# Optimization experiments

Measured on AMD Instinct MI355X. Metric: run time of the kernel, lower is better.

The kernel has to match this reference:

```python
import jax, jax.numpy as jnp
import numpy as np

N = 100000      # nodes
E = 320000      # edges
D = 128         # num_node_in_embeddings
DE = 256        # num_edge_in_embeddings = 2*D
NOBJ = 160
NREL = 27
BN_EPS = 1e-5   # eval-mode BatchNorm with running_mean=0, running_var=1


def setup_inputs() -> dict:
    key = jax.random.key(0)
    ks = jax.random.split(key, 24)
    f32 = jnp.float32
    def rn(k, shape, scale=0.05):
        return jax.random.normal(k, shape, f32) * scale
    return {
        "node_feats": jax.random.normal(ks[0], (N, D), f32),
        "edge_index": jax.random.randint(ks[1], (E, 2), 0, N),
        # GCNConv layers (W: [in,out], bias)
        "gcn1_W": rn(ks[2], (D, D // 2)), "gcn1_b": rn(ks[3], (D // 2,)),
        "gcn2_W": rn(ks[4], (D // 2, D)), "gcn2_b": rn(ks[5], (D,)),
        # edge attention (Linear(DE, D//2))
        "eattn_W": rn(ks[6], (DE, D // 2)), "eattn_b": rn(ks[7], (D // 2,)),
        # node attention (Linear(D, DE//2)) and indicator reduction (Linear(DE, DE//2))
        "nattn_W": rn(ks[8], (D, DE // 2)), "nattn_b": rn(ks[9], (DE // 2,)),
        "nred_W": rn(ks[10], (DE, DE // 2)), "nred_b": rn(ks[11], (DE // 2,)),
        # edge MLPs (1x1 Conv1d == Linear)
        "emlp1_W": rn(ks[12], (DE, DE // 2)), "emlp1_b": rn(ks[13], (DE // 2,)),
        "emlp2_W": rn(ks[14], (DE // 2, DE)), "emlp2_b": rn(ks[15], (DE,)),
        # node classification head
        "nlin1_W": rn(ks[16], (D, D // 2)),
        "nbn_g": jnp.ones((D // 2,), f32) + rn(ks[17], (D // 2,)),
        "nbn_b": rn(ks[18], (D // 2,)),
        "nlin2_W": rn(ks[19], (D // 2, NOBJ)),
        # edge classification head
        "elin1_W": rn(ks[20], (DE, DE // 2)),
        "ebn_g": jnp.ones((DE // 2,), f32) + rn(ks[21], (DE // 2,)),
        "ebn_b": rn(ks[22], (DE // 2,)),
        "elin2_W": rn(ks[23], (DE // 2, NREL)),
    }


def _seg_mean(vals, idx, n):
    # torch_scatter 'mean': sum / clamp(count, 1)
    s = jax.ops.segment_sum(vals, idx, num_segments=n)
    c = jax.ops.segment_sum(jnp.ones((vals.shape[0], 1), vals.dtype), idx, num_segments=n)
    return s / jnp.maximum(c, 1.0)


def _gcn_conv(x, src, dst, W, b, n):
    # PyG GCNConv, add_self_loops=True, symmetric normalization.
    lin = x @ W
    deg = jax.ops.segment_sum(jnp.ones((src.shape[0],), x.dtype), dst, num_segments=n) + 1.0
    dis = jax.lax.rsqrt(deg)                       # deg^{-1/2}, includes self-loop
    norm = dis[src] * dis[dst]                     # per-edge norm
    agg = jax.ops.segment_sum(lin[src] * norm[:, None], dst, num_segments=n)
    return agg + lin * (dis * dis)[:, None] + b    # self-loop term + bias


def _bn_eval(x, g, b):
    # eval-mode BatchNorm1d with running_mean=0, running_var=1
    return x * (g / jnp.sqrt(1.0 + BN_EPS)) + b


def reference(node_feats, edge_index, gcn1_W, gcn1_b, gcn2_W, gcn2_b,
              eattn_W, eattn_b, nattn_W, nattn_b, nred_W, nred_b,
              emlp1_W, emlp1_b, emlp2_W, emlp2_b,
              nlin1_W, nbn_g, nbn_b, nlin2_W,
              elin1_W, ebn_g, ebn_b, elin2_W):
    n = node_feats.shape[0]
    src = edge_index[:, 0]
    dst = edge_index[:, 1]

    # edge feature init: [subject, object - subject]  -> [E, DE]
    subj = node_feats[src]
    edge_feats = jnp.concatenate([subj, node_feats[dst] - subj], axis=1)

    # edge attention -> scatter-mean indicators over rows/cols -> node gate
    edge_ind = edge_feats @ eattn_W + eattn_b            # [E, D/2]
    row = _seg_mean(edge_ind, src, n)                    # [N, D/2]
    col = _seg_mean(edge_ind, dst, n)                    # [N, D/2]
    agg_edge_indicator = jax.nn.sigmoid(row * col)

    # two GCN layers (dropout is identity in eval mode)
    h = jax.nn.relu(_gcn_conv(node_feats, src, dst, gcn1_W, gcn1_b, n)) * agg_edge_indicator
    h = jax.nn.relu(_gcn_conv(h, src, dst, gcn2_W, gcn2_b, n))           # [N, D]

    # node attention -> per-edge gate
    node_ind = jax.nn.relu(h @ nattn_W + nattn_b)                        # [N, DE/2]
    econcat = jnp.concatenate([node_ind[src], node_ind[dst]], axis=1)    # [E, DE]
    agg_node_indicator = jax.nn.sigmoid(econcat @ nred_W + nred_b)       # [E, DE/2]

    # edge MLPs (1x1 convs == linears over edges)
    ef = jax.nn.relu(edge_feats @ emlp1_W + emlp1_b) * agg_node_indicator
    ef = jax.nn.relu(ef @ emlp2_W + emlp2_b)                             # [E, DE]

    # node head: linear -> BN(eval) -> leaky_relu(0.2) -> linear -> softmax over classes
    nx = jax.nn.leaky_relu(_bn_eval(h @ nlin1_W, nbn_g, nbn_b), 0.2)
    node_logits = jax.nn.softmax(nx @ nlin2_W, axis=1)                   # [N, NOBJ]

    # edge head: note original applies softmax on dim=1 of [1,E,NREL] -> over EDGES
    ex = jax.nn.leaky_relu(_bn_eval(ef @ elin1_W, ebn_g, ebn_b), 0.2)
    edge_logits = jax.nn.softmax(ex @ elin2_W, axis=0)                   # [E, NREL]

    return (node_logits, edge_logits)
```

## Files before the change

kernel.cpp:

```cpp
#include <hip/hip_runtime.h>

#define NN 100000
#define EE 320000

typedef unsigned int uint32;
typedef __attribute__((ext_vector_type(8))) short bf16x8;
typedef __attribute__((ext_vector_type(4))) float f32x4;
typedef __attribute__((ext_vector_type(16))) float f32x16;

__device__ __forceinline__ float4 ld4(const float* p){ return *(const float4*)p; }
__device__ __forceinline__ void st4(float* p, const float4 v){ *(float4*)p = v; }
__device__ __forceinline__ float sigm(float x){ return 1.f/(1.f + expf(-x)); }
__device__ __forceinline__ short f2b(float f){
  union { float f; uint32 u; } v; v.f = f;
  uint32 r = (v.u + 0x7FFFu + ((v.u>>16)&1u)) >> 16;
  return (short)r;
}
__device__ __forceinline__ float b2f(short s){
  union { uint32 u; float f; } v; v.u = ((uint32)(unsigned short)s) << 16; return v.f;
}

constexpr int EM_STORE=0, EM_BRELU=1, EM_BNLK=2;

template<int K,int NOUT,int EM>
__global__ __launch_bounds__(256) void gemm_k(
    const float* __restrict__ A,
    const float* __restrict__ W, const float* __restrict__ bias,
    const float* __restrict__ bng,
    float* __restrict__ C, int M)
{
  constexpr int CN = NOUT/16;
  __shared__ float As[16][68];
  __shared__ float Ws[16][NOUT];
  const int t  = threadIdx.x;
  const int tx = t & 15, ty = t >> 4;
  const int row0 = blockIdx.x * 64;

  float acc[4][CN];
  #pragma unroll
  for (int i=0;i<4;i++)
    #pragma unroll
    for (int j=0;j<CN;j++) acc[i][j]=0.f;

  const int r_st  = t >> 2;
  const int kq_st = (t & 3) * 4;

  for (int k0=0;k0<K;k0+=16) {
    {
      float4 v = make_float4(0.f,0.f,0.f,0.f);
      const int gr = row0 + r_st;
      if (gr < M) v = ld4(A + (size_t)gr*K + k0 + kq_st);
      As[kq_st+0][r_st]=v.x; As[kq_st+1][r_st]=v.y;
      As[kq_st+2][r_st]=v.z; As[kq_st+3][r_st]=v.w;
    }
    {
      constexpr int C4 = NOUT/4;
      for (int i=t;i<16*C4;i+=256){ int kk=i/C4, c4=(i%C4)*4;
        st4(&Ws[kk][c4], ld4(W + (size_t)(k0+kk)*NOUT + c4)); }
    }
    __syncthreads();
    #pragma unroll
    for (int kk=0;kk<16;kk++){
      float a0,a1,a2,a3;
      { const float4 av = *(const float4*)&As[kk][ty*4]; a0=av.x;a1=av.y;a2=av.z;a3=av.w; }
      float b[CN];
      if constexpr ((CN & 3) == 0) {
        #pragma unroll
        for (int j4=0;j4<CN;j4+=4){
          const float4 bv = *(const float4*)&Ws[kk][tx*CN+j4];
          b[j4]=bv.x;b[j4+1]=bv.y;b[j4+2]=bv.z;b[j4+3]=bv.w; }
      } else {
        #pragma unroll
        for (int j=0;j<CN;j++) b[j]=Ws[kk][tx*CN+j];
      }
      #pragma unroll
      for (int j=0;j<CN;j++){
        acc[0][j]=fmaf(a0,b[j],acc[0][j]);
        acc[1][j]=fmaf(a1,b[j],acc[1][j]);
        acc[2][j]=fmaf(a2,b[j],acc[2][j]);
        acc[3][j]=fmaf(a3,b[j],acc[3][j]);
      }
    }
    __syncthreads();
  }

  float sc[CN], sh[CN];
  if constexpr (EM==EM_BNLK) {
    const float r_ = rsqrtf(1.f + 1e-5f);
    #pragma unroll
    for (int j=0;j<CN;j++){ int c=tx*CN+j; sc[j]=bng[c]*r_; sh[j]=bias[c]; }
  }
  #pragma unroll
  for (int i=0;i<4;i++){
    const int r  = row0 + ty*4+i;
    if (r >= M) continue;
    #pragma unroll
    for (int j=0;j<CN;j++){
      const int c = tx*CN+j;
      float v = acc[i][j];
      if constexpr (EM==EM_BRELU) v = fmaxf(v + bias[c], 0.f);
      else if constexpr (EM==EM_BNLK){ float x = fmaf(v, sc[j], sh[j]); v = (x>0.f)? x : 0.2f*x; }
      C[(size_t)r*NOUT + c] = v;
    }
  }
}

__global__ void k_hist(const int* __restrict__ eidx, int* cntS, int* cntD, int E){
  int e = blockIdx.x*256+threadIdx.x; if (e>=E) return;
  atomicAdd(&cntS[eidx[2*e]], 1);
  atomicAdd(&cntD[eidx[2*e+1]], 1);
}
__global__ void k_scan_sum(const int* __restrict__ cnt, int* bsum, int n){
  __shared__ int red[256];
  const int b=blockIdx.x, t=threadIdx.x;
  int s=0;
  for (int i=b*1024+t; i<n && i<(b+1)*1024; i+=256) s += cnt[i];
  red[t]=s; __syncthreads();
  for (int o=128;o;o>>=1){ if(t<o) red[t]+=red[t+o]; __syncthreads(); }
  if (t==0) bsum[b]=red[0];
}
__global__ void k_scan_top(int* bsum, int nb){
  __shared__ int sh[256];
  const int t=threadIdx.x;
  int v=(t<nb)?bsum[t]:0;
  sh[t]=v; __syncthreads();
  for (int o=1;o<256;o<<=1){
    int u=0; if(t>=o) u=sh[t-o];
    __syncthreads();
    sh[t]+=u;
    __syncthreads();
  }
  if (t<nb) bsum[t]=sh[t]-v;
}
__global__ void k_scan_out(const int* __restrict__ cnt, const int* __restrict__ bofs,
                           int* __restrict__ off, int n){
  __shared__ int sh[256];
  const int b=blockIdx.x, t=threadIdx.x;
  const int base=b*1024+t*4;
  int c0=0,c1=0,c2=0,c3=0;
  if(base+0<n)c0=cnt[base+0];
  if(base+1<n)c1=cnt[base+1];
  if(base+2<n)c2=cnt[base+2];
  if(base+3<n)c3=cnt[base+3];
  int s=c0+c1+c2+c3;
  sh[t]=s; __syncthreads();
  int v=s;
  for (int o=1;o<256;o<<=1){
    int u=0; if(t>=o) u=sh[t-o];
    __syncthreads();
    sh[t]+=u;
    __syncthreads();
  }
  const int tofs = sh[t]-v + bofs[b];
  if(base+0<n) off[base+0]=tofs;
  if(base+1<n) off[base+1]=tofs+c0;
  if(base+2<n) off[base+2]=tofs+c0+c1;
  if(base+3<n) off[base+3]=tofs+c0+c1+c2;
}
__global__ void k_copyoff(const int* __restrict__ off, int* __restrict__ cur, int n){
  int i=blockIdx.x*256+threadIdx.x;
  if (i<n) cur[i]=off[i];
}
__global__ void k_setend(int* offS, int* offD, int n, int E){
  if (threadIdx.x==0 && blockIdx.x==0){ offS[n]=E; offD[n]=E; }
}
__global__ void k_fill(const int* __restrict__ eidx, int* curS, int* curD,
                       int* __restrict__ csrS, int* __restrict__ csrD, int E){
  int e=blockIdx.x*256+threadIdx.x; if (e>=E) return;
  const int s=eidx[2*e], d=eidx[2*e+1];
  csrS[atomicAdd(&curS[s],1)] = d;
  csrD[atomicAdd(&curD[d],1)] = s;
}
__global__ void k_dis(const int* __restrict__ cntD, float* __restrict__ dis, int n){
  int i=blockIdx.x*256+threadIdx.x; if(i>=n)return;
  dis[i]=rsqrtf((float)cntD[i]+1.f);
}

__global__ void k_wprep(const float* __restrict__ eattnW, const float* __restrict__ gcn1W,
                        float* __restrict__ Wcat){
  int idx=blockIdx.x*256+threadIdx.x; if (idx>=128*192) return;
  int k=idx/192, c=idx-k*192;
  float v;
  if (c<64)       v = eattnW[(size_t)(128+k)*64 + c];
  else if (c<128) v = eattnW[(size_t)k*64 + (c-64)] - eattnW[(size_t)(128+k)*64 + (c-64)];
  else            v = gcn1W[(size_t)k*64 + (c-128)];
  Wcat[idx]=v;
}

template<int NC>
__global__ void k_gather(const float* __restrict__ src, int stride, int colbase,
                         const int* __restrict__ off, const int* __restrict__ csr,
                         float* __restrict__ out, int n){
  constexpr int TPN = NC/4;
  const int t=threadIdx.x;
  const int node = blockIdx.x*(256/TPN) + t/TPN; if (node>=n) return;
  const int cq = (t%TPN)*4;
  const int j1=off[node+1];
  float4 acc = make_float4(0.f,0.f,0.f,0.f);
  for (int j=off[node]; j<j1; ++j){
    const float4 v = ld4(src + (size_t)csr[j]*stride + colbase + cq);
    acc.x+=v.x; acc.y+=v.y; acc.z+=v.z; acc.w+=v.w;
  }
  st4(out + (size_t)node*NC + cq, acc);
}

__global__ void k_aei3(const float* __restrict__ TUL, const float* __restrict__ Q,
                       const float* __restrict__ S, const int* __restrict__ cntS,
                       const int* __restrict__ cntD, const float* __restrict__ bias,
                       float* __restrict__ aei, int n){
  int idx=blockIdx.x*256+threadIdx.x; if (idx>=n*16) return;
  const int i=idx>>4, cq=(idx&15)*4;
  const float cS=(float)cntS[i], cD=(float)cntD[i];
  const float iS=1.f/fmaxf(cS,1.f), iD=1.f/fmaxf(cD,1.f);
  const float* tul = TUL + (size_t)i*192;
  const float4 T4=ld4(tul+cq), U4=ld4(tul+64+cq);
  const float4 Q4=ld4(Q+(size_t)i*64+cq), S4=ld4(S+(size_t)i*64+cq), b4=ld4(bias+cq);
  float4 o;
  o.x=sigm(((cS*(U4.x+b4.x)+Q4.x)*iS) * ((cD*(T4.x+b4.x)+S4.x)*iD));
  o.y=sigm(((cS*(U4.y+b4.y)+Q4.y)*iS) * ((cD*(T4.y+b4.y)+S4.y)*iD));
  o.z=sigm(((cS*(U4.z+b4.z)+Q4.z)*iS) * ((cD*(T4.z+b4.z)+S4.z)*iD));
  o.w=sigm(((cS*(U4.w+b4.w)+Q4.w)*iS) * ((cD*(T4.w+b4.w)+S4.w)*iD));
  st4(aei + (size_t)i*64 + cq, o);
}

template<int NC, bool AEI>
__global__ void k_gcnagg(const float* __restrict__ lin, int stride, int colbase,
                         const int* __restrict__ off, const int* __restrict__ csr,
                         const float* __restrict__ dis, const float* __restrict__ aei,
                         const float* __restrict__ bias, float* __restrict__ h, int n){
  constexpr int TPN = NC/4;
  const int t=threadIdx.x;
  const int node = blockIdx.x*(256/TPN) + t/TPN; if (node>=n) return;
  const int cq = (t%TPN)*4;
  const int j1=off[node+1];
  float4 acc = make_float4(0.f,0.f,0.f,0.f);
  for (int j=off[node]; j<j1; ++j){
    const int s=csr[j];
    const float w=dis[s];
    const float4 v = ld4(lin + (size_t)s*stride + colbase + cq);
    acc.x=fmaf(v.x,w,acc.x); acc.y=fmaf(v.y,w,acc.y);
    acc.z=fmaf(v.z,w,acc.z); acc.w=fmaf(v.w,w,acc.w);
  }
  const float dn=dis[node], d2=dn*dn;
  const float4 own=ld4(lin + (size_t)node*stride + colbase + cq), b4=ld4(bias+cq);
  float4 o;
  o.x=fmaxf(fmaf(acc.x,dn,fmaf(own.x,d2,b4.x)),0.f);
  o.y=fmaxf(fmaf(acc.y,dn,fmaf(own.y,d2,b4.y)),0.f);
  o.z=fmaxf(fmaf(acc.z,dn,fmaf(own.z,d2,b4.z)),0.f);
  o.w=fmaxf(fmaf(acc.w,dn,fmaf(own.w,d2,b4.w)),0.f);
  if (AEI){ const float4 m=ld4(aei+(size_t)node*NC+cq); o.x*=m.x;o.y*=m.y;o.z*=m.z;o.w*=m.w; }
  st4(h + (size_t)node*NC + cq, o);
}

__global__ void k_twtg(const float* __restrict__ Wa, const float* __restrict__ Wb,
                       short* __restrict__ Wt, int K, int N, int NP, int rowoff, int krot){
  int idx = blockIdx.x*256 + threadIdx.x;
  if (idx >= NP*K) return;
  int nn = idx / K, k = idx - nn*K;
  int ks = k + krot; if (ks >= K) ks -= K;
  float v = 0.f;
  if (nn < N){
    v = Wa[(size_t)(ks+rowoff)*N + nn];
    if (Wb) v -= Wb[(size_t)(ks+rowoff)*N + nn];
  }
  Wt[idx] = f2b(v);
}

template<int KTOT, int NT>
__device__ __forceinline__ void mm32(
    const short* __restrict__ Wt,
    short (*As)[258], short (*Bs)[28],
    int t, int lane, int w, f32x16* acc)
{
  constexpr int STEPS = KTOT/16;
  constexpr int NC = NT*32;
  const int lane31 = lane & 31, kh = lane >> 5;
  const int arow = w*32 + lane31;
  const bool act = (t < NC*2);
  const int col = t >> 1, half = t & 1;
  const short* wp = Wt + (size_t)col*KTOT + half*8;
  #pragma unroll
  for (int ks=0; ks<STEPS; ++ks){
    if (act) *(float4*)&Bs[col][half*8] = *(const float4*)(wp + ks*16);
    __syncthreads();
    const bf16x8 a = *(const bf16x8*)&As[arow][ks*16 + kh*8];
    #pragma unroll
    for (int ct=0; ct<NT; ++ct){
      const bf16x8 b = *(const bf16x8*)&Bs[ct*32 + lane31][kh*8];
      acc[ct] = __builtin_amdgcn_mfma_f32_32x32x16_bf16(a, b, acc[ct], 0, 0, 0);
    }
    __syncthreads();
  }
}

__device__ __forceinline__ int rowof(int reg, int kh){
  return (reg & 3) + ((reg >> 2) << 3) + (kh << 2);
}

__device__ __forceinline__ void storePA(short* __restrict__ dst, int cb, int n0, int n,
                                        int w, int kh, int lane31, const f32x16* acc){
  #pragma unroll
  for (int ct=0;ct<4;ct++){
    #pragma unroll
    for (int reg=0;reg<16;reg++){
      const int rr = n0 + w*32 + rowof(reg,kh);
      if (rr < n) dst[(size_t)rr*256 + cb + ct*32 + lane31] = f2b(acc[ct][reg]);
    }
  }
}

__global__ __launch_bounds__(256) void k_pa(
  const float* __restrict__ niB, const float* __restrict__ nf,
  const short* __restrict__ wt_p1, const short* __restrict__ wt_p2,
  const short* __restrict__ wt_a1, const short* __restrict__ wt_a2,
  short* __restrict__ PAs, short* __restrict__ PAd, int n)
{
  __shared__ short As[128][258];
  __shared__ short Bs[128][28];
  const int t = threadIdx.x, lane = t & 63, w = t >> 6;
  const int lane31 = lane & 31, kh = lane >> 5;
  const int n0 = blockIdx.x * 128;
  const int srow = t >> 1, shalf = t & 1;
  const int grow = n0 + srow;

  {
    short* dst = &As[srow][shalf*64];
    if (grow < n){
      const float* src = niB + (size_t)grow*128 + shalf*64;
      #pragma unroll
      for (int p=0;p<8;p++){
        float4 u=ld4(src+p*8), v=ld4(src+p*8+4);
        bf16x8 o;
        o[0]=f2b(u.x);o[1]=f2b(u.y);o[2]=f2b(u.z);o[3]=f2b(u.w);
        o[4]=f2b(v.x);o[5]=f2b(v.y);o[6]=f2b(v.z);o[7]=f2b(v.w);
        *(bf16x8*)(dst+p*8)=o;
      }
    } else {
      #pragma unroll
      for (int p=0;p<8;p++) *(bf16x8*)(dst+p*8) = (bf16x8)0;
    }
  }
  f32x16 acc[4];
  #pragma unroll
  for (int j=0;j<4;j++) acc[j]=(f32x16)(0.f);
  mm32<128,4>(wt_p1, As, Bs, t, lane, w, acc);
  storePA(PAs, 0, n0, n, w, kh, lane31, acc);
  #pragma unroll
  for (int j=0;j<4;j++) acc[j]=(f32x16)(0.f);
  mm32<128,4>(wt_p2, As, Bs, t, lane, w, acc);
  storePA(PAd, 0, n0, n, w, kh, lane31, acc);
  __syncthreads();

  {
    short* dst = &As[srow][shalf*64];
    if (grow < n){
      const float* src = nf + (size_t)grow*128 + shalf*64;
      #pragma unroll
      for (int p=0;p<8;p++){
        float4 u=ld4(src+p*8), v=ld4(src+p*8+4);
        bf16x8 o;
        o[0]=f2b(u.x);o[1]=f2b(u.y);o[2]=f2b(u.z);o[3]=f2b(u.w);
        o[4]=f2b(v.x);o[5]=f2b(v.y);o[6]=f2b(v.z);o[7]=f2b(v.w);
        *(bf16x8*)(dst+p*8)=o;
      }
    } else {
      #pragma unroll
      for (int p=0;p<8;p++) *(bf16x8*)(dst+p*8) = (bf16x8)0;
    }
  }
  #pragma unroll
  for (int j=0;j<4;j++) acc[j]=(f32x16)(0.f);
  mm32<128,4>(wt_a1, As, Bs, t, lane, w, acc);
  storePA(PAs, 128, n0, n, w, kh, lane31, acc);
  #pragma unroll
  for (int j=0;j<4;j++) acc[j]=(f32x16)(0.f);
  mm32<128,4>(wt_a2, As, Bs, t, lane, w, acc);
  storePA(PAd, 128, n0, n, w, kh, lane31, acc);
}

__global__ __launch_bounds__(256) void k_edge(
  const short* __restrict__ PAs, const short* __restrict__ PAd,
  const int* __restrict__ eidx,
  const float* __restrict__ nredb, const float* __restrict__ e1b,
  const short* __restrict__ wt_e2, const float* __restrict__ e2b,
  const short* __restrict__ wt_l1, const float* __restrict__ ebng, const float* __restrict__ ebnb,
  const short* __restrict__ wt_l2,
  float* __restrict__ elog)
{
  __shared__ short As[128][258];
  __shared__ short Bs[128][28];
  const int t = threadIdx.x, lane = t & 63, w = t >> 6;
  const int lane31 = lane & 31, kh = lane >> 5;
  const int row0 = blockIdx.x * 128;

  {
    const int srow = t >> 1, sseg = t & 1;
    const int e = row0 + srow;
    const int s = eidx[2*e], d = eidx[2*e+1];
    const short* ps = PAs + (size_t)s*256;
    const short* pd = PAd + (size_t)d*256;
    #pragma unroll
    for (int c0=0;c0<64;c0+=8){
      const int c = sseg*64 + c0;
      const bf16x8 p1 = *(const bf16x8*)(ps + c);
      const bf16x8 p2 = *(const bf16x8*)(pd + c);
      const bf16x8 a1 = *(const bf16x8*)(ps + 128 + c);
      const bf16x8 a2 = *(const bf16x8*)(pd + 128 + c);
      const float4 bg0=ld4(nredb+c), bg1=ld4(nredb+c+4);
      const float4 be0=ld4(e1b+c),   be1=ld4(e1b+c+4);
      const float bg[8]={bg0.x,bg0.y,bg0.z,bg0.w,bg1.x,bg1.y,bg1.z,bg1.w};
      const float be[8]={be0.x,be0.y,be0.z,be0.w,be1.x,be1.y,be1.z,be1.w};
      bf16x8 o;
      #pragma unroll
      for (int j=0;j<8;j++){
        const float g = sigm(b2f(p1[j]) + b2f(p2[j]) + bg[j]);
        const float v = fmaxf(b2f(a1[j]) + b2f(a2[j]) + be[j], 0.f) * g;
        o[j] = f2b(v);
      }
      *(bf16x8*)&As[srow][c] = o;
    }
  }

  f32x16 acc[4];
  #pragma unroll
  for (int j=0;j<4;j++) acc[j]=(f32x16)(0.f);
  mm32<128,4>(wt_e2, As, Bs, t, lane, w, acc);
  #pragma unroll
  for (int ct=0;ct<4;ct++){
    const int col = ct*32 + lane31;
    const float bb = e2b[col];
    #pragma unroll
    for (int reg=0;reg<16;reg++)
      As[w*32 + rowof(reg,kh)][128+col] = f2b(fmaxf(acc[ct][reg] + bb, 0.f));
  }
  #pragma unroll
  for (int j=0;j<4;j++) acc[j]=(f32x16)(0.f);
  mm32<128,4>(wt_e2 + (size_t)128*128, As, Bs, t, lane, w, acc);
  #pragma unroll
  for (int ct=0;ct<4;ct++){
    const int col = ct*32 + lane31;
    const float bb = e2b[128+col];
    #pragma unroll
    for (int reg=0;reg<16;reg++)
      As[w*32 + rowof(reg,kh)][col] = f2b(fmaxf(acc[ct][reg] + bb, 0.f));
  }

  #pragma unroll
  for (int j=0;j<4;j++) acc[j]=(f32x16)(0.f);
  mm32<256,4>(wt_l1, As, Bs, t, lane, w, acc);
  {
    const float r_ = rsqrtf(1.f + 1e-5f);
    #pragma unroll
    for (int ct=0;ct<4;ct++){
      const int col = ct*32 + lane31;
      const float sc = ebng[col]*r_, sh = ebnb[col];
      #pragma unroll
      for (int reg=0;reg<16;reg++){
        const float x = fmaf(acc[ct][reg], sc, sh);
        As[w*32 + rowof(reg,kh)][col] = f2b((x>0.f)? x : 0.2f*x);
      }
    }
  }

  f32x16 acc5 = (f32x16)(0.f);
  mm32<128,1>(wt_l2, As, Bs, t, lane, w, &acc5);

  float* Lb = (float*)&As[0][0];
  if (lane31 < 27){
    #pragma unroll
    for (int reg=0;reg<16;reg++)
      Lb[(w*32 + rowof(reg,kh))*28 + lane31] = acc5[reg];
  }
  __syncthreads();
  for (int i=t; i<128*27; i+=256){
    int rr = i/27, cc = i - rr*27;
    elog[(size_t)(row0+rr)*27 + cc] = Lb[rr*28 + cc];
  }
}

__global__ __launch_bounds__(256) void k_softmax_row(float* __restrict__ x, int M){
  const int wave = threadIdx.x>>6, lane = threadIdx.x&63;
  const int r = blockIdx.x*4 + wave; if (r>=M) return;
  float* p = x + (size_t)r*160;
  float v0 = p[lane], v1 = p[64+lane];
  float v2 = (lane<32)? p[128+lane] : -3.4e38f;
  float m = fmaxf(fmaxf(v0,v1),v2);
  for (int o=32;o;o>>=1) m = fmaxf(m, __shfl_xor(m,o));
  float e0=expf(v0-m), e1=expf(v1-m), e2=(lane<32)?expf(v2-m):0.f;
  float s=e0+e1+e2;
  for (int o=32;o;o>>=1) s += __shfl_xor(s,o);
  float inv = 1.f/s;
  p[lane]=e0*inv; p[64+lane]=e1*inv; if(lane<32)p[128+lane]=e2*inv;
}
__global__ void k_colmax(const float* __restrict__ x, uint32* __restrict__ cmax_u, int E){
  __shared__ float red[8][32];
  const int t=threadIdx.x, col=t&31, seg=t>>5;
  float m = -3.4e38f;
  if (col < 27)
    for (int r = blockIdx.x*8 + seg; r < E; r += gridDim.x*8)
      m = fmaxf(m, x[(size_t)r*27+col]);
  red[seg][col]=m; __syncthreads();
  if (t<32){
    float mm=red[0][t];
    #pragma unroll
    for (int s2=1;s2<8;s2++) mm=fmaxf(mm,red[s2][t]);
    if (t<27){
      uint32 u=__float_as_uint(mm);
      u = (u&0x80000000u)? ~u : (u|0x80000000u);
      atomicMax(&cmax_u[t], u);
    }
  }
}
__global__ void k_colfix(const uint32* __restrict__ cmax_u, float* __restrict__ cmaxf){
  int t=threadIdx.x; if (t>=27) return;
  uint32 u=cmax_u[t];
  cmaxf[t] = (u&0x80000000u)? __uint_as_float(u&0x7FFFFFFFu) : __uint_as_float(~u);
}
__global__ void k_colsum(const float* __restrict__ x, const float* __restrict__ cmaxf,
                         float* __restrict__ csum, int E){
  __shared__ float red[8][32];
  const int t=threadIdx.x, col=t&31, seg=t>>5;
  float s = 0.f;
  if (col < 27){
    const float cm = cmaxf[col];
    for (int r = blockIdx.x*8 + seg; r < E; r += gridDim.x*8)
      s += expf(x[(size_t)r*27+col] - cm);
  }
  red[seg][col]=s; __syncthreads();
  if (t<32){
    float ss=red[0][t];
    #pragma unroll
    for (int s2=1;s2<8;s2++) ss+=red[s2][t];
    if (t<27) atomicAdd(&csum[t], ss);
  }
}
__global__ void k_colnorm(float* __restrict__ x, const float* __restrict__ cmaxf,
                          const float* __restrict__ csum, int E){
  int idx=blockIdx.x*256+threadIdx.x;
  if (idx >= E*27) return;
  int c = idx - (idx/27)*27;
  x[idx] = expf(x[idx]-cmaxf[c]) / csum[c];
}

extern "C" void kernel_launch(void* const* d_in, const int* in_sizes, int n_in,
                              void* d_out, int out_size, void* d_ws, size_t ws_size,
                              hipStream_t stream)
{
  const float* nf     = (const float*)d_in[0];
  const int*   eidx   = (const int*)  d_in[1];
  const float* gcn1W  = (const float*)d_in[2];
  const float* gcn1b  = (const float*)d_in[3];
  const float* gcn2W  = (const float*)d_in[4];
  const float* gcn2b  = (const float*)d_in[5];
  const float* eattnW = (const float*)d_in[6];
  const float* eattnb = (const float*)d_in[7];
  const float* nattnW = (const float*)d_in[8];
  const float* nattnb = (const float*)d_in[9];
  const float* nredW  = (const float*)d_in[10];
  const float* nredb  = (const float*)d_in[11];
  const float* emlp1W = (const float*)d_in[12];
  const float* emlp1b = (const float*)d_in[13];
  const float* emlp2W = (const float*)d_in[14];
  const float* emlp2b = (const float*)d_in[15];
  const float* nlin1W = (const float*)d_in[16];
  const float* nbng   = (const float*)d_in[17];
  const float* nbnb   = (const float*)d_in[18];
  const float* nlin2W = (const float*)d_in[19];
  const float* elin1W = (const float*)d_in[20];
  const float* ebng   = (const float*)d_in[21];
  const float* ebnb   = (const float*)d_in[22];
  const float* elin2W = (const float*)d_in[23];
  (void)in_sizes; (void)n_in; (void)out_size; (void)ws_size;

  const int N = NN, E = EE;
  float* out  = (float*)d_out;
  float* nlog = out;
  float* elog = out + (size_t)N*160;

  float* ws   = (float*)d_ws;
  float* h2   = ws;
  float* lin2 = ws + (size_t)N*128;
  float* Q    = lin2;
  float* S    = lin2 + (size_t)N*64;
  float* niB  = lin2;
  float* nx   = lin2;
  float* TUL  = ws + (size_t)N*256;
  float* h1   = ws + (size_t)N*448;
  short* PAs  = (short*)TUL;
  short* PAd  = PAs + (size_t)N*256;
  float* aei  = ws + (size_t)N*512;
  float* dis  = ws + (size_t)N*576;
  float* smalls = ws + (size_t)N*577;
  float* Wcat = smalls + 128;
  int*   ip   = (int*)(Wcat + 24576);
  int* cntS = ip;
  int* cntD = ip + N;
  int* offS = ip + 2*N;
  int* offD = ip + 3*N + 64;
  int* curS = ip + 4*N + 128;
  int* curD = ip + 5*N + 128;
  int* csrS = ip + 6*N + 128;
  int* csrD = ip + 6*N + 128 + E;
  int* bsum = ip + 6*N + 128 + 2*E;
  short* wtb  = (short*)(bsum + 256);
  short* wt_p1 = wtb;
  short* wt_p2 = wtb + 16384;
  short* wt_a1 = wtb + 32768;
  short* wt_a2 = wtb + 49152;
  short* wt_e2 = wtb + 65536;
  short* wt_l1 = wtb + 98304;
  short* wt_l2 = wtb + 131072;

  const int NB1024 = (N + 1023)/1024;

  k_twtg<<<64, 256,0,stream>>>(nredW,  nullptr, wt_p1, 128,128,128, 0,   0);
  k_twtg<<<64, 256,0,stream>>>(nredW,  nullptr, wt_p2, 128,128,128, 128, 0);
  k_twtg<<<64, 256,0,stream>>>(emlp1W, emlp1W+(size_t)128*128, wt_a1, 128,128,128, 0, 0);
  k_twtg<<<64, 256,0,stream>>>(emlp1W, nullptr, wt_a2, 128,128,128, 128, 0);
  k_twtg<<<128,256,0,stream>>>(emlp2W, nullptr, wt_e2, 128,256,256, 0,   0);
  k_twtg<<<128,256,0,stream>>>(elin1W, nullptr, wt_l1, 256,128,128, 0, 128);
  k_twtg<<<16, 256,0,stream>>>(elin2W, nullptr, wt_l2, 128,27, 32,  0,   0);
  k_wprep<<<96,256,0,stream>>>(eattnW, gcn1W, Wcat);

  (void)hipMemsetAsync(cntS, 0, 2*(size_t)N*sizeof(int), stream);
  k_hist<<<(E+255)/256,256,0,stream>>>(eidx, cntS, cntD, E);
  k_scan_sum<<<NB1024,256,0,stream>>>(cntS, bsum, N);
  k_scan_top<<<1,256,0,stream>>>(bsum, NB1024);
  k_scan_out<<<NB1024,256,0,stream>>>(cntS, bsum, offS, N);
  k_scan_sum<<<NB1024,256,0,stream>>>(cntD, bsum, N);
  k_scan_top<<<1,256,0,stream>>>(bsum, NB1024);
  k_scan_out<<<NB1024,256,0,stream>>>(cntD, bsum, offD, N);
  k_setend<<<1,64,0,stream>>>(offS, offD, N, E);
  k_copyoff<<<(N+255)/256,256,0,stream>>>(offS, curS, N);
  k_copyoff<<<(N+255)/256,256,0,stream>>>(offD, curD, N);
  k_fill<<<(E+255)/256,256,0,stream>>>(eidx, curS, curD, csrS, csrD, E);
  k_dis<<<(N+255)/256,256,0,stream>>>(cntD, dis, N);

  gemm_k<128,192,EM_STORE><<<(N+63)/64,256,0,stream>>>(nf, Wcat, nullptr, nullptr, TUL, N);

  k_gather<64><<<(N+15)/16,256,0,stream>>>(TUL, 192, 0,  offS, csrS, Q, N);
  k_gather<64><<<(N+15)/16,256,0,stream>>>(TUL, 192, 64, offD, csrD, S, N);
  k_aei3<<<(N*16+255)/256,256,0,stream>>>(TUL, Q, S, cntS, cntD, eattnb, aei, N);

  k_gcnagg<64,true><<<(N+15)/16,256,0,stream>>>(TUL, 192, 128, offD, csrD, dis, aei, gcn1b, h1, N);

  gemm_k<64,128,EM_STORE><<<(N+63)/64,256,0,stream>>>(h1, gcn2W, nullptr, nullptr, lin2, N);
  k_gcnagg<128,false><<<(N+7)/8,256,0,stream>>>(lin2, 128, 0, offD, csrD, dis, nullptr, gcn2b, h2, N);

  gemm_k<128,128,EM_BRELU><<<(N+63)/64,256,0,stream>>>(h2, nattnW, nattnb, nullptr, niB, N);

  k_pa<<<(N+127)/128,256,0,stream>>>(niB, nf, wt_p1, wt_p2, wt_a1, wt_a2, PAs, PAd, N);

  k_edge<<<E/128,256,0,stream>>>(
      PAs, PAd, eidx,
      nredb, emlp1b, wt_e2, emlp2b,
      wt_l1, ebng, ebnb, wt_l2, elog);

  gemm_k<128,64,EM_BNLK><<<(N+63)/64,256,0,stream>>>(h2, nlin1W, nbnb, nbng, nx, N);
  gemm_k<64,160,EM_STORE><<<(N+63)/64,256,0,stream>>>(nx, nlin2W, nullptr, nullptr, nlog, N);
  k_softmax_row<<<(N+3)/4,256,0,stream>>>(nlog, N);

  (void)hipMemsetAsync(smalls, 0, 96*sizeof(float), stream);
  k_colmax<<<1024,256,0,stream>>>(elog, (uint32*)smalls, E);
  k_colfix<<<1,32,0,stream>>>((const uint32*)smalls, smalls+64);
  k_colsum<<<1024,256,0,stream>>>(elog, smalls+64, smalls+32, E);
  k_colnorm<<<(E*27+255)/256,256,0,stream>>>(elog, smalls+64, smalls+32, E);
}
```

Baseline: 1.063 ms.

## Halve row tiles in k_pa/k_edge and split MFMA columns across wave pairs

The MFMA helper now has each pair of waves share a 32-row slab and split the output columns between them, so blocks cover 64 rows instead of 128. This halves shared memory per block and accumulator registers per wave, which should allow more blocks per CU and more grid parallelism in k_pa and k_edge. k_pa also stages its outputs through a shared-memory buffer so that global stores are coalesced 16-byte writes instead of scattered 2-byte ones. In exchange, weight tiles are reloaded into shared memory once per 64 rows rather than per 128, and there are extra barriers. In the final 27-column layer half the waves do redundant work.

```diff
diff --git a/kernel.cpp b/kernel.cpp
--- a/kernel.cpp
+++ b/kernel.cpp
@@ -266,17 +266,18 @@
   Wt[idx] = f2b(v);
 }
 
-template<int KTOT, int NT>
+template<int KTOT, int NCOLTOT>
 __device__ __forceinline__ void mm32(
     const short* __restrict__ Wt,
     short (*As)[258], short (*Bs)[28],
     int t, int lane, int w, f32x16* acc)
 {
   constexpr int STEPS = KTOT/16;
-  constexpr int NC = NT*32;
+  constexpr int NT = (NCOLTOT>=64)? NCOLTOT/64 : 1;
   const int lane31 = lane & 31, kh = lane >> 5;
-  const int arow = w*32 + lane31;
-  const bool act = (t < NC*2);
+  const int arow = (w>>1)*32 + lane31;
+  const int colbase = (NCOLTOT>=64)? (w&1)*(NCOLTOT/2) : 0;
+  const bool act = (t < NCOLTOT*2);
   const int col = t >> 1, half = t & 1;
   const short* wp = Wt + (size_t)col*KTOT + half*8;
   #pragma unroll
@@ -286,7 +287,7 @@
     const bf16x8 a = *(const bf16x8*)&As[arow][ks*16 + kh*8];
     #pragma unroll
     for (int ct=0; ct<NT; ++ct){
-      const bf16x8 b = *(const bf16x8*)&Bs[ct*32 + lane31][kh*8];
+      const bf16x8 b = *(const bf16x8*)&Bs[colbase + ct*32 + lane31][kh*8];
       acc[ct] = __builtin_amdgcn_mfma_f32_32x32x16_bf16(a, b, acc[ct], 0, 0, 0);
     }
     __syncthreads();
@@ -295,18 +296,6 @@
 
 __device__ __forceinline__ int rowof(int reg, int kh){
   return (reg & 3) + ((reg >> 2) << 3) + (kh << 2);
-}
-
-__device__ __forceinline__ void storePA(short* __restrict__ dst, int cb, int n0, int n,
-                                        int w, int kh, int lane31, const f32x16* acc){
-  #pragma unroll
-  for (int ct=0;ct<4;ct++){
-    #pragma unroll
-    for (int reg=0;reg<16;reg++){
-      const int rr = n0 + w*32 + rowof(reg,kh);
-      if (rr < n) dst[(size_t)rr*256 + cb + ct*32 + lane31] = f2b(acc[ct][reg]);
-    }
-  }
 }
 
 __global__ __launch_bounds__(256) void k_pa(
@@ -315,67 +304,71 @@
   const short* __restrict__ wt_a1, const short* __restrict__ wt_a2,
   short* __restrict__ PAs, short* __restrict__ PAd, int n)
 {
-  __shared__ short As[128][258];
+  __shared__ short As[64][258];
+  __shared__ short Out[64][136];
   __shared__ short Bs[128][28];
   const int t = threadIdx.x, lane = t & 63, w = t >> 6;
   const int lane31 = lane & 31, kh = lane >> 5;
-  const int n0 = blockIdx.x * 128;
-  const int srow = t >> 1, shalf = t & 1;
+  const int n0 = blockIdx.x * 64;
+  const int srow = t >> 2, q = t & 3;
   const int grow = n0 + srow;
 
-  {
-    short* dst = &As[srow][shalf*64];
-    if (grow < n){
-      const float* src = niB + (size_t)grow*128 + shalf*64;
-      #pragma unroll
-      for (int p=0;p<8;p++){
-        float4 u=ld4(src+p*8), v=ld4(src+p*8+4);
-        bf16x8 o;
-        o[0]=f2b(u.x);o[1]=f2b(u.y);o[2]=f2b(u.z);o[3]=f2b(u.w);
-        o[4]=f2b(v.x);o[5]=f2b(v.y);o[6]=f2b(v.z);o[7]=f2b(v.w);
-        *(bf16x8*)(dst+p*8)=o;
-      }
-    } else {
-      #pragma unroll
-      for (int p=0;p<8;p++) *(bf16x8*)(dst+p*8) = (bf16x8)0;
-    }
-  }
-  f32x16 acc[4];
-  #pragma unroll
-  for (int j=0;j<4;j++) acc[j]=(f32x16)(0.f);
-  mm32<128,4>(wt_p1, As, Bs, t, lane, w, acc);
-  storePA(PAs, 0, n0, n, w, kh, lane31, acc);
-  #pragma unroll
-  for (int j=0;j<4;j++) acc[j]=(f32x16)(0.f);
-  mm32<128,4>(wt_p2, As, Bs, t, lane, w, acc);
-  storePA(PAd, 0, n0, n, w, kh, lane31, acc);
-  __syncthreads();
-
-  {
-    short* dst = &As[srow][shalf*64];
-    if (grow < n){
-      const float* src = nf + (size_t)grow*128 + shalf*64;
-      #pragma unroll
-      for (int p=0;p<8;p++){
-        float4 u=ld4(src+p*8), v=ld4(src+p*8+4);
-        bf16x8 o;
-        o[0]=f2b(u.x);o[1]=f2b(u.y);o[2]=f2b(u.z);o[3]=f2b(u.w);
-        o[4]=f2b(v.x);o[5]=f2b(v.y);o[6]=f2b(v.z);o[7]=f2b(v.w);
-        *(bf16x8*)(dst+p*8)=o;
-      }
-    } else {
-      #pragma unroll
-      for (int p=0;p<8;p++) *(bf16x8*)(dst+p*8) = (bf16x8)0;
-    }
-  }
-  #pragma unroll
-  for (int j=0;j<4;j++) acc[j]=(f32x16)(0.f);
-  mm32<128,4>(wt_a1, As, Bs, t, lane, w, acc);
-  storePA(PAs, 128, n0, n, w, kh, lane31, acc);
-  #pragma unroll
-  for (int j=0;j<4;j++) acc[j]=(f32x16)(0.f);
-  mm32<128,4>(wt_a2, As, Bs, t, lane, w, acc);
-  storePA(PAd, 128, n0, n, w, kh, lane31, acc);
+#define STAGE_SRC(SRC)                                                       \
+  {                                                                          \
+    short* dst = &As[srow][q*32];                                            \
+    if (grow < n){                                                           \
+      const float* src = (SRC) + (size_t)grow*128 + q*32;                    \
+      _Pragma("unroll")                                                      \
+      for (int p=0;p<4;p++){                                                 \
+        float4 u=ld4(src+p*8), v=ld4(src+p*8+4);                             \
+        bf16x8 o;                                                            \
+        o[0]=f2b(u.x);o[1]=f2b(u.y);o[2]=f2b(u.z);o[3]=f2b(u.w);             \
+        o[4]=f2b(v.x);o[5]=f2b(v.y);o[6]=f2b(v.z);o[7]=f2b(v.w);             \
+        *(bf16x8*)(dst+p*8)=o;                                               \
+      }                                                                      \
+    } else {                                                                 \
+      _Pragma("unroll")                                                      \
+      for (int p=0;p<4;p++) *(bf16x8*)(dst+p*8) = (bf16x8)0;                 \
+    }                                                                        \
+  }
+
+#define OUT_AND_STORE(DST, CB)                                               \
+  {                                                                          \
+    const int colbase = (w&1)*64;                                            \
+    _Pragma("unroll")                                                        \
+    for (int ct=0;ct<2;ct++){                                                \
+      _Pragma("unroll")                                                      \
+      for (int reg=0;reg<16;reg++)                                           \
+        Out[(w>>1)*32 + rowof(reg,kh)][colbase + ct*32 + lane31] =           \
+            f2b(acc[ct][reg]);                                               \
+    }                                                                        \
+    __syncthreads();                                                         \
+    if (grow < n){                                                           \
+      const float* srcp = (const float*)&Out[srow][q*32];                    \
+      float* dstp = (float*)((DST) + (size_t)grow*256 + (CB) + q*32);        \
+      _Pragma("unroll")                                                      \
+      for (int p=0;p<4;p++) st4(dstp + p*4, ld4(srcp + p*4));                \
+    }                                                                        \
+    __syncthreads();                                                         \
+  }
+
+  f32x16 acc[2];
+  STAGE_SRC(niB);
+  acc[0]=(f32x16)(0.f); acc[1]=(f32x16)(0.f);
+  mm32<128,128>(wt_p1, As, Bs, t, lane, w, acc);
+  OUT_AND_STORE(PAs, 0);
+  acc[0]=(f32x16)(0.f); acc[1]=(f32x16)(0.f);
+  mm32<128,128>(wt_p2, As, Bs, t, lane, w, acc);
+  OUT_AND_STORE(PAd, 0);
+  STAGE_SRC(nf);
+  acc[0]=(f32x16)(0.f); acc[1]=(f32x16)(0.f);
+  mm32<128,128>(wt_a1, As, Bs, t, lane, w, acc);
+  OUT_AND_STORE(PAs, 128);
+  acc[0]=(f32x16)(0.f); acc[1]=(f32x16)(0.f);
+  mm32<128,128>(wt_a2, As, Bs, t, lane, w, acc);
+  OUT_AND_STORE(PAd, 128);
+#undef STAGE_SRC
+#undef OUT_AND_STORE
 }
 
 __global__ __launch_bounds__(256) void k_edge(
@@ -387,21 +380,21 @@
   const short* __restrict__ wt_l2,
   float* __restrict__ elog)
 {
-  __shared__ short As[128][258];
+  __shared__ short As[64][258];
   __shared__ short Bs[128][28];
   const int t = threadIdx.x, lane = t & 63, w = t >> 6;
   const int lane31 = lane & 31, kh = lane >> 5;
-  const int row0 = blockIdx.x * 128;
+  const int row0 = blockIdx.x * 64;
 
   {
-    const int srow = t >> 1, sseg = t & 1;
+    const int srow = t >> 2, q = t & 3;
     const int e = row0 + srow;
     const int s = eidx[2*e], d = eidx[2*e+1];
     const short* ps = PAs + (size_t)s*256;
     const short* pd = PAd + (size_t)d*256;
     #pragma unroll
-    for (int c0=0;c0<64;c0+=8){
-      const int c = sseg*64 + c0;
+    for (int c0=0;c0<32;c0+=8){
+      const int c = q*32 + c0;
       const bf16x8 p1 = *(const bf16x8*)(ps + c);
       const bf16x8 p2 = *(const bf16x8*)(pd + c);
       const bf16x8 a1 = *(const bf16x8*)(ps + 128 + c);
@@ -421,58 +414,55 @@
     }
   }
 
-  f32x16 acc[4];
+  f32x16 acc[2];
+  acc[0]=(f32x16)(0.f); acc[1]=(f32x16)(0.f);
+  mm32<128,128>(wt_e2, As, Bs, t, lane, w, acc);
   #pragma unroll
-  for (int j=0;j<4;j++) acc[j]=(f32x16)(0.f);
-  mm32<128,4>(wt_e2, As, Bs, t, lane, w, acc);
+  for (int ct=0;ct<2;ct++){
+    const int col = (w&1)*64 + ct*32 + lane31;
+    const float bb = e2b[col];
+    #pragma unroll
+    for (int reg=0;reg<16;reg++)
+      As[(w>>1)*32 + rowof(reg,kh)][128+col] = f2b(fmaxf(acc[ct][reg] + bb, 0.f));
+  }
+  acc[0]=(f32x16)(0.f); acc[1]=(f32x16)(0.f);
+  mm32<128,128>(wt_e2 + (size_t)128*128, As, Bs, t, lane, w, acc);
   #pragma unroll
-  for (int ct=0;ct<4;ct++){
-    const int col = ct*32 + lane31;
-    const float bb = e2b[col];
+  for (int ct=0;ct<2;ct++){
+    const int col = (w&1)*64 + ct*32 + lane31;
+    const float bb = e2b[128+col];
     #pragma unroll
     for (int reg=0;reg<16;reg++)
-      As[w*32 + rowof(reg,kh)][128+col] = f2b(fmaxf(acc[ct][reg] + bb, 0.f));
-  }
-  #pragma unroll
-  for (int j=0;j<4;j++) acc[j]=(f32x16)(0.f);
-  mm32<128,4>(wt_e2 + (size_t)128*128, As, Bs, t, lane, w, acc);
-  #pragma unroll
-  for (int ct=0;ct<4;ct++){
-    const int col = ct*32 + lane31;
-    const float bb = e2b[128+col];
-    #pragma unroll
-    for (int reg=0;reg<16;reg++)
-      As[w*32 + rowof(reg,kh)][col] = f2b(fmaxf(acc[ct][reg] + bb, 0.f));
-  }
-
-  #pragma unroll
-  for (int j=0;j<4;j++) acc[j]=(f32x16)(0.f);
-  mm32<256,4>(wt_l1, As, Bs, t, lane, w, acc);
+      As[(w>>1)*32 + rowof(reg,kh)][col] = f2b(fmaxf(acc[ct][reg] + bb, 0.f));
+  }
+
+  acc[0]=(f32x16)(0.f); acc[1]=(f32x16)(0.f);
+  mm32<256,128>(wt_l1, As, Bs, t, lane, w, acc);
   {
     const float r_ = rsqrtf(1.f + 1e-5f);
     #pragma unroll
-    for (int ct=0;ct<4;ct++){
-      const int col = ct*32 + lane31;
+    for (int ct=0;ct<2;ct++){
+      const int col = (w&1)*64 + ct*32 + lane31;
       const float sc = ebng[col]*r_, sh = ebnb[col];
       #pragma unroll
       for (int reg=0;reg<16;reg++){
         const float x = fmaf(acc[ct][reg], sc, sh);
-        As[w*32 + rowof(reg,kh)][col] = f2b((x>0.f)? x : 0.2f*x);
+        As[(w>>1)*32 + rowof(reg,kh)][col] = f2b((x>0.f)? x : 0.2f*x);
       }
     }
   }
 
   f32x16 acc5 = (f32x16)(0.f);
-  mm32<128,1>(wt_l2, As, Bs, t, lane, w, &acc5);
+  mm32<128,32>(wt_l2, As, Bs, t, lane, w, &acc5);
 
   float* Lb = (float*)&As[0][0];
-  if (lane31 < 27){
+  if ((w&1)==0 && lane31 < 27){
     #pragma unroll
     for (int reg=0;reg<16;reg++)
-      Lb[(w*32 + rowof(reg,kh))*28 + lane31] = acc5[reg];
+      Lb[((w>>1)*32 + rowof(reg,kh))*28 + lane31] = acc5[reg];
   }
   __syncthreads();
-  for (int i=t; i<128*27; i+=256){
+  for (int i=t; i<64*27; i+=256){
     int rr = i/27, cc = i - rr*27;
     elog[(size_t)(row0+rr)*27 + cc] = Lb[rr*28 + cc];
   }
@@ -649,9 +639,9 @@
 
   gemm_k<128,128,EM_BRELU><<<(N+63)/64,256,0,stream>>>(h2, nattnW, nattnb, nullptr, niB, N);
 
-  k_pa<<<(N+127)/128,256,0,stream>>>(niB, nf, wt_p1, wt_p2, wt_a1, wt_a2, PAs, PAd, N);
-
-  k_edge<<<E/128,256,0,stream>>>(
+  k_pa<<<(N+63)/64,256,0,stream>>>(niB, nf, wt_p1, wt_p2, wt_a1, wt_a2, PAs, PAd, N);
+
+  k_edge<<<E/64,256,0,stream>>>(
       PAs, PAd, eidx,
       nredb, emlp1b, wt_e2, emlp2b,
       wt_l1, ebng, ebnb, wt_l2, elog);
```

Result: no change. 1.074 ms (+1.0%).
